# Optimization experiments

Hardware: AMD Instinct MI355X
Metric: run time of the kernel (lower is better)

The kernel has to match this reference:

```python
import jax, jax.numpy as jnp
import numpy as np

NUM_ITERS = 3
NUM_SLOTS = 8
D = 128
MLP_HIDDEN = 128
EPS = 1e-8
LN_EPS = 1e-5
B, N = 64, 4096


def _layer_norm(x, g, b):
    m = jnp.mean(x, axis=-1, keepdims=True)
    v = jnp.mean(jnp.square(x - m), axis=-1, keepdims=True)
    return (x - m) * jax.lax.rsqrt(v + LN_EPS) * g + b


def setup_inputs() -> dict:
    key = jax.random.key(0)
    ks = jax.random.split(key, 16)
    s = 1.0 / np.sqrt(D)
    inp = {
        "x": jax.random.normal(ks[0], (B, N, D), jnp.float32),
        "slots_init": jax.random.normal(ks[1], (B, NUM_SLOTS, D), jnp.float32),
        "Wq": jax.random.normal(ks[2], (D, D), jnp.float32) * s,
        "bq": jnp.zeros((D,), jnp.float32),
        "Wk": jax.random.normal(ks[3], (D, D), jnp.float32) * s,
        "bk": jnp.zeros((D,), jnp.float32),
        "Wv": jax.random.normal(ks[4], (D, D), jnp.float32) * s,
        "bv": jnp.zeros((D,), jnp.float32),
        "g_in": jnp.ones((D,), jnp.float32), "b_in": jnp.zeros((D,), jnp.float32),
        "g_slot": jnp.ones((D,), jnp.float32), "b_slot": jnp.zeros((D,), jnp.float32),
        "g_mlp": jnp.ones((D,), jnp.float32), "b_mlp": jnp.zeros((D,), jnp.float32),
        "W1": jax.random.normal(ks[5], (MLP_HIDDEN, D), jnp.float32) * s,
        "b1": jnp.zeros((MLP_HIDDEN,), jnp.float32),
        "W2": jax.random.normal(ks[6], (D, MLP_HIDDEN), jnp.float32) * (1.0 / np.sqrt(MLP_HIDDEN)),
        "b2": jnp.zeros((D,), jnp.float32),
        "W_ih": jax.random.normal(ks[7], (3 * D, D), jnp.float32) * s,
        "W_hh": jax.random.normal(ks[8], (3 * D, D), jnp.float32) * s,
        "b_ih": jnp.zeros((3 * D,), jnp.float32),
        "b_hh": jnp.zeros((3 * D,), jnp.float32),
    }
    return inp


def _gru_cell(x, h, W_ih, W_hh, b_ih, b_hh):
    # torch.nn.GRUCell semantics
    gi = x @ W_ih.T + b_ih          # [.., 3D]
    gh = h @ W_hh.T + b_hh
    i_r, i_z, i_n = jnp.split(gi, 3, axis=-1)
    h_r, h_z, h_n = jnp.split(gh, 3, axis=-1)
    r = jax.nn.sigmoid(i_r + h_r)
    z = jax.nn.sigmoid(i_z + h_z)
    n = jnp.tanh(i_n + r * h_n)
    return (1.0 - z) * n + z * h


def reference(x, slots_init, Wq, bq, Wk, bk, Wv, bv, g_in, b_in, g_slot, b_slot,
              g_mlp, b_mlp, W1, b1, W2, b2, W_ih, W_hh, b_ih, b_hh):
    xn = _layer_norm(x, g_in, b_in)                 # [B,N,D]
    keys = xn @ Wk.T + bk                            # [B,N,D]
    values = xn @ Wv.T + bv                          # [B,N,D]
    scale = D ** -0.5
    slots = slots_init                               # [B,K,D]
    for _ in range(NUM_ITERS):
        prev = slots
        s = _layer_norm(slots, g_slot, b_slot)
        q = s @ Wq.T + bq                            # [B,K,D]
        logits = jnp.einsum('bid,bkd->bik', q, keys) * scale  # [B,K,N]
        attn = jax.nn.softmax(logits, axis=1)        # softmax over SLOT axis
        attn = attn + EPS
        attn = attn / jnp.sum(attn, axis=-1, keepdims=True)
        updates = jnp.einsum('bkd,bik->bid', values, attn)     # [B,K,D]
        slots = _gru_cell(updates.reshape(-1, D), prev.reshape(-1, D),
                          W_ih, W_hh, b_ih, b_hh).reshape(x.shape[0], -1, D)
        h = jax.nn.relu(_layer_norm(slots, g_mlp, b_mlp) @ W1.T + b1)
        slots = slots + (h @ W2.T + b2)
    return slots
```

## Files before the change

kernel.cpp:

```cpp
#include <hip/hip_runtime.h>
#include <hip/hip_bf16.h>

#define B_ 64
#define N_ 4096
#define KS 8
#define NCH 32
#define TP 136
#define LNEPS 1e-5f
#define EPSA 1e-8f
#define SCALE 0.08838834764831845f

typedef short short8  __attribute__((ext_vector_type(8)));
typedef short short4v __attribute__((ext_vector_type(4)));
typedef float f32x4   __attribute__((ext_vector_type(4)));
typedef float f32x2   __attribute__((ext_vector_type(2)));

__device__ __forceinline__ unsigned short f2bf(float f) {
  union { float f; unsigned u; } v; v.f = f;
  unsigned r = v.u + 0x7fffu + ((v.u >> 16) & 1u);
  return (unsigned short)(r >> 16);
}
__device__ __forceinline__ float bflo(unsigned u) {
  union { unsigned u; float f; } c; c.u = u << 16; return c.f;
}
__device__ __forceinline__ float bfhi(unsigned u) {
  union { unsigned u; float f; } c; c.u = u & 0xffff0000u; return c.f;
}
__device__ __forceinline__ float sigmf(float x) { return 1.f / (1.f + __expf(-x)); }

__device__ __forceinline__ void pkfma_lo(f32x2 &d, f32x2 f, f32x2 p2) {
  asm("v_pk_fma_f32 %0, %1, %2, %0 op_sel_hi:[1,0,1]" : "+v"(d) : "v"(f), "v"(p2));
}
__device__ __forceinline__ void pkfma_hi(f32x2 &d, f32x2 f, f32x2 p2) {
  asm("v_pk_fma_f32 %0, %1, %2, %0 op_sel:[0,1,0] op_sel_hi:[1,1,1]" : "+v"(d) : "v"(f), "v"(p2));
}

__global__ __launch_bounds__(256) void prep_all(
    const float* __restrict__ Wih, const float* __restrict__ Whh,
    const float* __restrict__ Wq,  const float* __restrict__ Wv,
    const float* __restrict__ W1,  const float* __restrict__ W2,
    float* __restrict__ WgT, float* __restrict__ WqT,
    float* __restrict__ WvT, float* __restrict__ W1T, float* __restrict__ W2T,
    const float* __restrict__ slots_in, const float* __restrict__ g_slot, const float* __restrict__ b_slot,
    const float* __restrict__ bq,
    const float* __restrict__ Wk, const float* __restrict__ bk,
    float* __restrict__ qt, float* __restrict__ qc,
    const float* __restrict__ x, const float* __restrict__ g_in, const float* __restrict__ b_in,
    unsigned short* __restrict__ xn)
{
  __shared__ float sarr[128];
  __shared__ float qarr[128];
  const int bb = blockIdx.x, t = threadIdx.x;

  if (bb < 640) {
    int id = bb * 256 + t;
    if (id < 98304) {
      int d = id / 768, j = id % 768;
      WgT[id] = (j < 384) ? Wih[j*128 + d] : Whh[(j-384)*128 + d];
    } else if (id < 114688) {
      int k = id - 98304; WqT[k] = Wq[(k % 128) * 128 + k / 128];
    } else if (id < 131072) {
      int k = id - 114688; WvT[k] = Wv[(k % 128) * 128 + k / 128];
    } else if (id < 147456) {
      int k = id - 131072; W1T[k] = W1[(k % 128) * 128 + k / 128];
    } else if (id < 163840) {
      int k = id - 147456; W2T[k] = W2[(k % 128) * 128 + k / 128];
    }
    return;
  }

  if (bb < 1152) {
    int row = bb - 640;
    if (t < 64) {
      float a = slots_in[row*128 + t], b = slots_in[row*128 + 64 + t];
      float s = a + b, s2 = a*a + b*b;
      #pragma unroll
      for (int st = 1; st < 64; st <<= 1) { s += __shfl_xor(s, st); s2 += __shfl_xor(s2, st); }
      float mean = s * (1.f/128.f);
      float rstd = rsqrtf(s2 * (1.f/128.f) - mean*mean + LNEPS);
      sarr[t]    = (a - mean) * rstd * g_slot[t]    + b_slot[t];
      sarr[t+64] = (b - mean) * rstd * g_slot[t+64] + b_slot[t+64];
    }
    __syncthreads();
    if (t < 128) {
      float a = bq[t];
      for (int d = 0; d < 128; d++) a += sarr[d] * Wq[t*128 + d];
      qarr[t] = a;
    }
    __syncthreads();
    if (t < 128) {
      float a = 0.f;
      for (int j = 0; j < 128; j++) a += qarr[j] * Wk[j*128 + t];
      qt[row*128 + t] = a * SCALE;
    }
    if (t < 64) {
      float c = qarr[t]*bk[t] + qarr[t+64]*bk[t+64];
      #pragma unroll
      for (int st = 1; st < 64; st <<= 1) c += __shfl_xor(c, st);
      if (t == 0) qc[row] = c * SCALE;
    }
    return;
  }

  {
    const int w = t >> 6, lane = t & 63;
    const int half = lane >> 5, sl = lane & 31;
    const size_t row0 = (size_t)(bb - 1152) * 128 + w * 32 + half;
    float4 gg = *(const float4*)(g_in + sl*4);
    float4 bv4 = *(const float4*)(b_in + sl*4);
    for (int i = 0; i < 16; i++) {
      size_t row = row0 + i*2;
      float4 v = *(const float4*)(x + row*128 + sl*4);
      float s  = v.x + v.y + v.z + v.w;
      float s2 = v.x*v.x + v.y*v.y + v.z*v.z + v.w*v.w;
      #pragma unroll
      for (int st = 1; st < 32; st <<= 1) { s += __shfl_xor(s, st); s2 += __shfl_xor(s2, st); }
      float mean = s * (1.f/128.f);
      float rstd = rsqrtf(s2*(1.f/128.f) - mean*mean + LNEPS);
      unsigned short h0 = f2bf((v.x - mean)*rstd*gg.x + bv4.x);
      unsigned short h1 = f2bf((v.y - mean)*rstd*gg.y + bv4.y);
      unsigned short h2 = f2bf((v.z - mean)*rstd*gg.z + bv4.z);
      unsigned short h3 = f2bf((v.w - mean)*rstd*gg.w + bv4.w);
      uint2 pk;
      pk.x = (unsigned)h0 | ((unsigned)h1 << 16);
      pk.y = (unsigned)h2 | ((unsigned)h3 << 16);
      *(uint2*)(xn + row*128 + sl*4) = pk;
    }
  }
}

__global__ __launch_bounds__(256) void attn_kernel(
    const unsigned short* __restrict__ xn,
    const float* __restrict__ qt, const float* __restrict__ qc,
    float* __restrict__ Upart, float* __restrict__ Spart)
{
  __shared__ union ShMem {
    unsigned short xt[4][16][TP];
    float ured[4][8][128];
  } sh;
  __shared__ __align__(16) float pb[4][16][8];
  __shared__ float sred[4][8];

  const int tid = threadIdx.x;
  const int w = tid >> 6, lane = tid & 63;
  const int chunk = blockIdx.x, batch = blockIdx.y;
  const int m = lane & 15, quad = lane >> 4;

  short8 afrag[4];
  if (m < KS) {
    const float* qp = qt + (batch*KS + m)*128 + quad*8;
    #pragma unroll
    for (int kc = 0; kc < 4; kc++) {
      short8 a;
      #pragma unroll
      for (int j = 0; j < 8; j++) a[j] = (short)f2bf(qp[kc*32 + j]);
      afrag[kc] = a;
    }
  } else {
    #pragma unroll
    for (int kc = 0; kc < 4; kc++) {
      short8 a;
      #pragma unroll
      for (int j = 0; j < 8; j++) a[j] = 0;
      afrag[kc] = a;
    }
  }
  float creg[4];
  #pragma unroll
  for (int r = 0; r < 4; r++) creg[r] = qc[batch*KS + ((quad*4 + r) & 7)];

  const int tb = (chunk*4 + w) * 32;
  const unsigned short* xp0 = xn + (size_t)(batch*N_ + tb + m)*128;
  const unsigned short* xp1 = xp0 + 16*128;
  short8 bfA[4], bfB[4];
  #pragma unroll
  for (int kc = 0; kc < 4; kc++) bfA[kc] = *(const short8*)(xp0 + kc*32 + quad*8);
  #pragma unroll
  for (int kc = 0; kc < 4; kc++) bfB[kc] = *(const short8*)(xp1 + kc*32 + quad*8);

  f32x2 u01[8];
  #pragma unroll
  for (int i = 0; i < 8; i++) { u01[i].x = 0.f; u01[i].y = 0.f; }
  float sAcc[4] = {0.f, 0.f, 0.f, 0.f};

  #pragma unroll
  for (int g = 0; g < 2; g++) {
    short8* bf = g ? bfB : bfA;

    #pragma unroll
    for (int kc = 0; kc < 4; kc++)
      *(short8*)&sh.xt[w][m][kc*32 + quad*8] = bf[kc];

    f32x4 acc = {0.f, 0.f, 0.f, 0.f};
    #pragma unroll
    for (int kc = 0; kc < 4; kc++)
      acc = __builtin_amdgcn_mfma_f32_16x16x32_bf16(afrag[kc], bf[kc], acc, 0, 0, 0);
    float l[4], o[4];
    #pragma unroll
    for (int r = 0; r < 4; r++) l[r] = acc[r] + creg[r];
    #pragma unroll
    for (int r = 0; r < 4; r++) o[r] = __shfl_xor(l[r], 16);
    float mx = fmaxf(fmaxf(fmaxf(l[0], l[1]), fmaxf(l[2], l[3])),
                     fmaxf(fmaxf(o[0], o[1]), fmaxf(o[2], o[3])));
    float e0 = __expf(l[0]-mx), e1 = __expf(l[1]-mx), e2 = __expf(l[2]-mx), e3 = __expf(l[3]-mx);
    float den = e0+e1+e2+e3 + __expf(o[0]-mx)+__expf(o[1]-mx)+__expf(o[2]-mx)+__expf(o[3]-mx);
    float rd = 1.f / den;
    float p0 = e0*rd + EPSA, p1 = e1*rd + EPSA, p2 = e2*rd + EPSA, p3 = e3*rd + EPSA;
    if (lane < 32) {
      float4 pv; pv.x = p0; pv.y = p1; pv.z = p2; pv.w = p3;
      *(float4*)&pb[w][m][quad*4] = pv;
    }

    #pragma unroll
    for (int t = 0; t < 16; t++) {
      f32x2 pA01 = *(const f32x2*)&pb[w][t][0];
      f32x2 pA23 = *(const f32x2*)&pb[w][t][2];
      f32x2 pB01 = *(const f32x2*)&pb[w][t][4];
      f32x2 pB23 = *(const f32x2*)&pb[w][t][6];
      unsigned vp = *(const unsigned*)&sh.xt[w][t][lane*2];
      f32x2 f; f.x = bflo(vp); f.y = bfhi(vp);
      pkfma_lo(u01[0], f, pA01); pkfma_hi(u01[1], f, pA01);
      pkfma_lo(u01[2], f, pA23); pkfma_hi(u01[3], f, pA23);
      pkfma_lo(u01[4], f, pB01); pkfma_hi(u01[5], f, pB01);
      pkfma_lo(u01[6], f, pB23); pkfma_hi(u01[7], f, pB23);
    }

    float sac[4] = {p0, p1, p2, p3};
    #pragma unroll
    for (int st = 1; st < 16; st <<= 1) {
      #pragma unroll
      for (int r = 0; r < 4; r++) sac[r] += __shfl_xor(sac[r], st);
    }
    #pragma unroll
    for (int r = 0; r < 4; r++) sAcc[r] += sac[r];
  }

  if (lane == 0)  { sred[w][0]=sAcc[0]; sred[w][1]=sAcc[1]; sred[w][2]=sAcc[2]; sred[w][3]=sAcc[3]; }
  if (lane == 16) { sred[w][4]=sAcc[0]; sred[w][5]=sAcc[1]; sred[w][6]=sAcc[2]; sred[w][7]=sAcc[3]; }

  __syncthreads();
  #pragma unroll
  for (int i = 0; i < 8; i++)
    *(f32x2*)&sh.ured[w][i][lane*2] = u01[i];
  __syncthreads();

  {
    const float* ur = &sh.ured[0][0][0];
    int i4 = tid * 4;
    float4 a = *(const float4*)(ur + i4);
    float4 b = *(const float4*)(ur + 1024 + i4);
    float4 c = *(const float4*)(ur + 2048 + i4);
    float4 d = *(const float4*)(ur + 3072 + i4);
    float4 o4;
    o4.x = a.x+b.x+c.x+d.x; o4.y = a.y+b.y+c.y+d.y;
    o4.z = a.z+b.z+c.z+d.z; o4.w = a.w+b.w+c.w+d.w;
    *(float4*)(Upart + (size_t)(batch*NCH + chunk)*1024 + i4) = o4;
    if (tid < 8)
      Spart[(batch*NCH + chunk)*8 + tid] =
        sred[0][tid] + sred[1][tid] + sred[2][tid] + sred[3][tid];
  }
}

__global__ __launch_bounds__(256) void update_kernel(
    const float* __restrict__ slots_in, float* __restrict__ slots_out,
    const float* __restrict__ Upart, const float* __restrict__ Spart,
    const float* __restrict__ WvT, const float* __restrict__ bv,
    const float* __restrict__ WgT,
    const float* __restrict__ b_ih, const float* __restrict__ b_hh,
    const float* __restrict__ g_mlp, const float* __restrict__ b_mlp,
    const float* __restrict__ W1T, const float* __restrict__ b1,
    const float* __restrict__ W2T, const float* __restrict__ b2,
    const float* __restrict__ g_slot, const float* __restrict__ b_slot,
    const float* __restrict__ WqT, const float* __restrict__ bq,
    const float* __restrict__ Wk, const float* __restrict__ bk,
    float* __restrict__ qt, float* __restrict__ qc)
{
  __shared__ float bu[128], su[128], hb[128];
  __shared__ float gg[768];
  __shared__ float s1[128], smv[128], hmv[128], s2v[128], sqv[128], qa[128];
  __shared__ float up2[2][128];
  __shared__ float stats[2], sSum;
  int row = blockIdx.x, t = threadIdx.x;
  int batch = row >> 3, slot = row & 7;
  const int col = t & 127, hf = t >> 7;

  {
    const float* Up = Upart + ((size_t)(batch*NCH + hf*16)*8 + slot)*128 + col;
    float ua = 0.f;
    #pragma unroll
    for (int c = 0; c < 16; c++) ua += Up[(size_t)c*1024];
    up2[hf][col] = ua;
  }
  if (t < NCH) {
    float sv = Spart[(batch*NCH + t)*8 + slot];
    #pragma unroll
    for (int st = 1; st < NCH; st <<= 1) sv += __shfl_xor(sv, st);
    if (t == 0) sSum = sv;
  }
  if (t >= 64 && t < 192) hb[t-64] = slots_in[row*128 + (t-64)];
  __syncthreads();
  if (t < 128) bu[t] = (up2[0][t] + up2[1][t]) / sSum;
  __syncthreads();
  {
    float a = hf ? 0.f : bv[col];
    const float* W = WvT + hf*64*128;
    const float* v = bu + hf*64;
    #pragma unroll 8
    for (int d = 0; d < 64; d++) a += v[d] * W[d*128 + col];
    __syncthreads();
    up2[hf][col] = a;
  }
  __syncthreads();
  if (t < 128) su[t] = up2[0][t] + up2[1][t];
  __syncthreads();
  {
    float a0 = b_ih[t];
    float a1 = (t < 128) ? b_ih[256+t] : b_hh[t-128];
    float a2 = b_hh[t+128];
    const float* v1p = (t < 128) ? su : hb;
    for (int d = 0; d < 128; d++) {
      float sd = su[d], hd = hb[d], vd = v1p[d];
      const float* wr = WgT + d*768 + t;
      a0 += sd * wr[0];
      a1 += vd * wr[256];
      a2 += hd * wr[512];
    }
    gg[t] = a0; gg[t+256] = a1; gg[t+512] = a2;
  }
  __syncthreads();
  if (t < 128) {
    float r = sigmf(gg[t] + gg[384+t]);
    float z = sigmf(gg[128+t] + gg[512+t]);
    float n = tanhf(gg[256+t] + r * gg[640+t]);
    s1[t] = (1.f - z)*n + z*hb[t];
  }
  __syncthreads();
  if (t < 64) {
    float a = s1[t], b = s1[t+64];
    float s = a + b, s2 = a*a + b*b;
    #pragma unroll
    for (int st = 1; st < 64; st <<= 1) { s += __shfl_xor(s, st); s2 += __shfl_xor(s2, st); }
    if (t == 0) { float mean = s*(1.f/128.f); stats[0] = mean;
                  stats[1] = rsqrtf(s2*(1.f/128.f) - mean*mean + LNEPS); }
  }
  __syncthreads();
  if (t < 128) smv[t] = (s1[t] - stats[0])*stats[1]*g_mlp[t] + b_mlp[t];
  __syncthreads();
  {
    float a = hf ? 0.f : b1[col];
    const float* W = W1T + hf*64*128;
    const float* v = smv + hf*64;
    #pragma unroll 8
    for (int d = 0; d < 64; d++) a += v[d] * W[d*128 + col];
    up2[hf][col] = a;
  }
  __syncthreads();
  if (t < 128) hmv[t] = fmaxf(up2[0][t] + up2[1][t], 0.f);
  __syncthreads();
  {
    float a = 0.f;
    const float* W = W2T + hf*64*128;
    const float* v = hmv + hf*64;
    #pragma unroll 8
    for (int d = 0; d < 64; d++) a += v[d] * W[d*128 + col];
    up2[hf][col] = a;
  }
  __syncthreads();
  if (t < 128) {
    float a = s1[t] + b2[t] + up2[0][t] + up2[1][t];
    s2v[t] = a;
    slots_out[row*128 + t] = a;
  }
  __syncthreads();
  if (t < 64) {
    float a = s2v[t], b = s2v[t+64];
    float s = a + b, s2 = a*a + b*b;
    #pragma unroll
    for (int st = 1; st < 64; st <<= 1) { s += __shfl_xor(s, st); s2 += __shfl_xor(s2, st); }
    if (t == 0) { float mean = s*(1.f/128.f); stats[0] = mean;
                  stats[1] = rsqrtf(s2*(1.f/128.f) - mean*mean + LNEPS); }
  }
  __syncthreads();
  if (t < 128) sqv[t] = (s2v[t] - stats[0])*stats[1]*g_slot[t] + b_slot[t];
  __syncthreads();
  {
    float a = hf ? 0.f : bq[col];
    const float* W = WqT + hf*64*128;
    const float* v = sqv + hf*64;
    #pragma unroll 8
    for (int d = 0; d < 64; d++) a += v[d] * W[d*128 + col];
    up2[hf][col] = a;
  }
  __syncthreads();
  if (t < 128) qa[t] = up2[0][t] + up2[1][t];
  __syncthreads();
  {
    float a = 0.f;
    const float* W = Wk + hf*64*128;
    const float* v = qa + hf*64;
    #pragma unroll 8
    for (int j = 0; j < 64; j++) a += v[j] * W[j*128 + col];
    up2[hf][col] = a;
  }
  __syncthreads();
  if (t < 128) qt[row*128 + t] = (up2[0][t] + up2[1][t]) * SCALE;
  if (t < 64) {
    float c = qa[t]*bk[t] + qa[t+64]*bk[t+64];
    #pragma unroll
    for (int st = 1; st < 64; st <<= 1) c += __shfl_xor(c, st);
    if (t == 0) qc[row] = c * SCALE;
  }
}

extern "C" void kernel_launch(void* const* d_in, const int* in_sizes, int n_in,
                              void* d_out, int out_size, void* d_ws, size_t ws_size,
                              hipStream_t stream) {
  const float* x          = (const float*)d_in[0];
  const float* slots_init = (const float*)d_in[1];
  const float* Wq   = (const float*)d_in[2];
  const float* bq   = (const float*)d_in[3];
  const float* Wk   = (const float*)d_in[4];
  const float* bk   = (const float*)d_in[5];
  const float* Wv   = (const float*)d_in[6];
  const float* bv   = (const float*)d_in[7];
  const float* g_in = (const float*)d_in[8];
  const float* b_in = (const float*)d_in[9];
  const float* g_slot = (const float*)d_in[10];
  const float* b_slot = (const float*)d_in[11];
  const float* g_mlp  = (const float*)d_in[12];
  const float* b_mlp  = (const float*)d_in[13];
  const float* W1   = (const float*)d_in[14];
  const float* b1   = (const float*)d_in[15];
  const float* W2   = (const float*)d_in[16];
  const float* b2   = (const float*)d_in[17];
  const float* Wih  = (const float*)d_in[18];
  const float* Whh  = (const float*)d_in[19];
  const float* b_ih = (const float*)d_in[20];
  const float* b_hh = (const float*)d_in[21];

  char* p = (char*)d_ws;
  unsigned short* xn = (unsigned short*)p; p += (size_t)B_*N_*128*2;
  float* qt    = (float*)p; p += (size_t)B_*KS*128*4;
  float* qc    = (float*)p; p += (size_t)B_*KS*4 + 2048;
  float* slots = (float*)p; p += (size_t)B_*KS*128*4;
  float* Upart = (float*)p; p += (size_t)B_*NCH*KS*128*4;
  float* Spart = (float*)p; p += (size_t)B_*NCH*KS*4 + 2048;
  float* WgT   = (float*)p; p += 98304*4;
  float* WqT   = (float*)p; p += 16384*4;
  float* WvT   = (float*)p; p += 16384*4;
  float* W1T   = (float*)p; p += 16384*4;
  float* W2T   = (float*)p; p += 16384*4;

  prep_all<<<3200, 256, 0, stream>>>(Wih, Whh, Wq, Wv, W1, W2,
      WgT, WqT, WvT, W1T, W2T,
      slots_init, g_slot, b_slot, bq, Wk, bk, qt, qc,
      x, g_in, b_in, xn);

  attn_kernel<<<dim3(NCH, B_), 256, 0, stream>>>(xn, qt, qc, Upart, Spart);
  update_kernel<<<512, 256, 0, stream>>>(slots_init, slots, Upart, Spart,
      WvT, bv, WgT, b_ih, b_hh, g_mlp, b_mlp, W1T, b1, W2T, b2,
      g_slot, b_slot, WqT, bq, Wk, bk, qt, qc);

  attn_kernel<<<dim3(NCH, B_), 256, 0, stream>>>(xn, qt, qc, Upart, Spart);
  update_kernel<<<512, 256, 0, stream>>>(slots, slots, Upart, Spart,
      WvT, bv, WgT, b_ih, b_hh, g_mlp, b_mlp, W1T, b1, W2T, b2,
      g_slot, b_slot, WqT, bq, Wk, bk, qt, qc);

  attn_kernel<<<dim3(NCH, B_), 256, 0, stream>>>(xn, qt, qc, Upart, Spart);
  update_kernel<<<512, 256, 0, stream>>>(slots, (float*)d_out, Upart, Spart,
      WvT, bv, WgT, b_ih, b_hh, g_mlp, b_mlp, W1T, b1, W2T, b2,
      g_slot, b_slot, WqT, bq, Wk, bk, qt, qc);

  (void)in_sizes; (void)n_in; (void)out_size; (void)ws_size;
}
```

Measured before the change: 377.0 us.

## Process four token groups per warp with double-buffered loads, halving chunks

Each warp now handles 64 tokens (four groups of 16) instead of 32, so the number of chunks per batch drops from 32 to 16. The next group's bf16 input fragments are prefetched into a second register buffer while the current group is processed. The per-group shuffle reduction of attention sums is deferred to a single reduction after the loop, and the finalize kernel reads half as many partial sums. The intent is less partial-sum traffic and reduction work and better load latency hiding, at the cost of fewer blocks (less parallelism) and more registers per thread.

```diff
diff --git a/kernel.cpp b/kernel.cpp
--- a/kernel.cpp
+++ b/kernel.cpp
@@ -4,7 +4,8 @@
 #define B_ 64
 #define N_ 4096
 #define KS 8
-#define NCH 32
+#define NCH 16
+#define NG 4
 #define TP 136
 #define LNEPS 1e-5f
 #define EPSA 1e-8f
@@ -169,14 +170,12 @@
   #pragma unroll
   for (int r = 0; r < 4; r++) creg[r] = qc[batch*KS + ((quad*4 + r) & 7)];
 
-  const int tb = (chunk*4 + w) * 32;
-  const unsigned short* xp0 = xn + (size_t)(batch*N_ + tb + m)*128;
-  const unsigned short* xp1 = xp0 + 16*128;
-  short8 bfA[4], bfB[4];
-  #pragma unroll
-  for (int kc = 0; kc < 4; kc++) bfA[kc] = *(const short8*)(xp0 + kc*32 + quad*8);
-  #pragma unroll
-  for (int kc = 0; kc < 4; kc++) bfB[kc] = *(const short8*)(xp1 + kc*32 + quad*8);
+  const int tb = (chunk*4 + w) * (NG*16);
+  const unsigned short* xpb = xn + (size_t)(batch*N_ + tb + m)*128 + quad*8;
+
+  short8 b0[4], b1[4];
+  #pragma unroll
+  for (int kc = 0; kc < 4; kc++) b0[kc] = *(const short8*)(xpb + kc*32);
 
   f32x2 u01[8];
   #pragma unroll
@@ -184,17 +183,24 @@
   float sAcc[4] = {0.f, 0.f, 0.f, 0.f};
 
   #pragma unroll
-  for (int g = 0; g < 2; g++) {
-    short8* bf = g ? bfB : bfA;
+  for (int g = 0; g < NG; g++) {
+    short8* bc = (g & 1) ? b1 : b0;
+    short8* bn = (g & 1) ? b0 : b1;
+
+    if (g + 1 < NG) {
+      const unsigned short* xq = xpb + (size_t)(g + 1) * 16 * 128;
+      #pragma unroll
+      for (int kc = 0; kc < 4; kc++) bn[kc] = *(const short8*)(xq + kc*32);
+    }
 
     #pragma unroll
     for (int kc = 0; kc < 4; kc++)
-      *(short8*)&sh.xt[w][m][kc*32 + quad*8] = bf[kc];
+      *(short8*)&sh.xt[w][m][kc*32 + quad*8] = bc[kc];
 
     f32x4 acc = {0.f, 0.f, 0.f, 0.f};
     #pragma unroll
     for (int kc = 0; kc < 4; kc++)
-      acc = __builtin_amdgcn_mfma_f32_16x16x32_bf16(afrag[kc], bf[kc], acc, 0, 0, 0);
+      acc = __builtin_amdgcn_mfma_f32_16x16x32_bf16(afrag[kc], bc[kc], acc, 0, 0, 0);
     float l[4], o[4];
     #pragma unroll
     for (int r = 0; r < 4; r++) l[r] = acc[r] + creg[r];
@@ -225,16 +231,14 @@
       pkfma_lo(u01[6], f, pB23); pkfma_hi(u01[7], f, pB23);
     }
 
-    float sac[4] = {p0, p1, p2, p3};
-    #pragma unroll
-    for (int st = 1; st < 16; st <<= 1) {
-      #pragma unroll
-      for (int r = 0; r < 4; r++) sac[r] += __shfl_xor(sac[r], st);
-    }
-    #pragma unroll
-    for (int r = 0; r < 4; r++) sAcc[r] += sac[r];
-  }
-
+    sAcc[0] += p0; sAcc[1] += p1; sAcc[2] += p2; sAcc[3] += p3;
+  }
+
+  #pragma unroll
+  for (int st = 1; st < 16; st <<= 1) {
+    #pragma unroll
+    for (int r = 0; r < 4; r++) sAcc[r] += __shfl_xor(sAcc[r], st);
+  }
   if (lane == 0)  { sred[w][0]=sAcc[0]; sred[w][1]=sAcc[1]; sred[w][2]=sAcc[2]; sred[w][3]=sAcc[3]; }
   if (lane == 16) { sred[w][4]=sAcc[0]; sred[w][5]=sAcc[1]; sred[w][6]=sAcc[2]; sred[w][7]=sAcc[3]; }
 
@@ -285,10 +289,10 @@
   const int col = t & 127, hf = t >> 7;
 
   {
-    const float* Up = Upart + ((size_t)(batch*NCH + hf*16)*8 + slot)*128 + col;
+    const float* Up = Upart + ((size_t)(batch*NCH + hf*8)*8 + slot)*128 + col;
     float ua = 0.f;
     #pragma unroll
-    for (int c = 0; c < 16; c++) ua += Up[(size_t)c*1024];
+    for (int c = 0; c < 8; c++) ua += Up[(size_t)c*1024];
     up2[hf][col] = ua;
   }
   if (t < NCH) {
```

After: 372.0 us. Within noise of the previous version (-1.3%).
